# Kernel optimization log

Measured on AMD Instinct MI355X. Metric: run time of the kernel, lower is better.

Reference implementation:

```python
import jax, jax.numpy as jnp
import numpy as np

N, C, H, W = 8, 64, 128, 128
K2 = 9  # 3x3 kernel
BN_EPS = 1e-5


def conv3x3(x, w):
    # x: [N,Ci,H,W], w: [Co,Ci,3,3], stride 1, padding 1, dilation 1
    return jax.lax.conv_general_dilated(
        x, w, window_strides=(1, 1), padding=((1, 1), (1, 1)),
        dimension_numbers=('NCHW', 'OIHW', 'NCHW'))


def deform_conv3x3(x, offset, w):
    # torchvision deform_conv2d v1 (no mask), stride 1, pad 1, dil 1, 1 group.
    # offset: [N, 2*K2, H, W] ordered (dy, dx) per kernel tap.
    n, c, h, wd = x.shape
    off = offset.reshape(n, K2, 2, h, wd)
    k = jnp.arange(3) - 1  # kernel tap displacements with pad=1
    ky, kx = jnp.meshgrid(k, k, indexing='ij')
    ky = ky.reshape(K2).astype(x.dtype)
    kx = kx.reshape(K2).astype(x.dtype)
    ys = jnp.arange(h, dtype=x.dtype)
    xs = jnp.arange(wd, dtype=x.dtype)
    # sampling positions: [N, K2, H, W]
    py = ys[None, None, :, None] + ky[None, :, None, None] + off[:, :, 0]
    px = xs[None, None, None, :] + kx[None, :, None, None] + off[:, :, 1]
    y0f = jnp.floor(py)
    x0f = jnp.floor(px)
    wy1 = py - y0f
    wx1 = px - x0f
    y0 = y0f.astype(jnp.int32)
    x0 = x0f.astype(jnp.int32)
    xflat = x.reshape(n, c, h * wd)

    def corner(yc, xc, wgt):
        valid = ((yc >= 0) & (yc < h) & (xc >= 0) & (xc < wd)).astype(x.dtype)
        idx = jnp.clip(yc, 0, h - 1) * wd + jnp.clip(xc, 0, wd - 1)  # [N,K2,H,W]
        gath = jax.vmap(lambda xf, i: jnp.take(xf, i.reshape(-1), axis=1)
                        .reshape(c, K2, h, wd))(xflat, idx)  # [N,C,K2,H,W]
        return gath * (wgt * valid)[:, None]

    samp = (corner(y0, x0, (1 - wy1) * (1 - wx1))
            + corner(y0, x0 + 1, (1 - wy1) * wx1)
            + corner(y0 + 1, x0, wy1 * (1 - wx1))
            + corner(y0 + 1, x0 + 1, wy1 * wx1))  # [N,C,K2,H,W]
    return jnp.einsum('nckhw,ock->nohw', samp, w.reshape(w.shape[0], c, K2))


def setup_inputs() -> dict:
    key = jax.random.key(0)
    ks = jax.random.split(key, 5)
    x = jax.random.normal(ks[0], (N, C, H, W), dtype=jnp.float32)
    # small offset-conv weights so predicted offsets stay within a few pixels
    w_off = jax.random.normal(ks[1], (2 * K2 + 9, C, 3, 3), dtype=jnp.float32) * 0.01
    w_def = jax.random.normal(ks[2], (C, C, 3, 3), dtype=jnp.float32) * (1.0 / np.sqrt(C * 9))
    w1 = jax.random.normal(ks[3], (K2, C, 3, 3), dtype=jnp.float32) * (1.0 / np.sqrt(C * 9))
    gamma = jnp.ones((K2,), jnp.float32)
    beta = jnp.zeros((K2,), jnp.float32)
    mean = jnp.zeros((K2,), jnp.float32)
    var = jnp.ones((K2,), jnp.float32)
    return {"x": x, "w_off": w_off, "w_def": w_def, "w1": w1,
            "gamma": gamma, "beta": beta, "mean": mean, "var": var}


def reference(x, w_off, w_def, w1, gamma, beta, mean, var):
    off_filter = conv3x3(x, w_off)            # [N, 27, H, W]
    offset = off_filter[:, :2 * K2]           # [N, 18, H, W]
    filt = off_filter[:, -K2:]                # [N, 9, H, W]
    out = deform_conv3x3(x, offset, w_def)    # [N, C, H, W]
    xr = x + out
    h = conv3x3(xr, w1)                       # [N, 9, H, W]
    # BatchNorm2d (inference form with running stats)
    h = (h - mean[None, :, None, None]) * jax.lax.rsqrt(var[None, :, None, None] + BN_EPS)
    h = h * gamma[None, :, None, None] + beta[None, :, None, None]
    h = jnp.maximum(h, 0.0)
    return (h, filt)
```

## Files before the change

kernel.cpp:

```cpp
#include <hip/hip_runtime.h>
#include <cmath>

#define H_ 128
#define W_ 128
#define HW_ 16384
#define C_ 64
#define N_ 8
#define BN_EPS 1e-5f

typedef __attribute__((ext_vector_type(8))) short short8;
typedef __attribute__((ext_vector_type(4))) float float4_;

__device__ inline short f2bf(float f) {
    unsigned u = __builtin_bit_cast(unsigned, f);
    u += 0x7fffu + ((u >> 16) & 1u);
    return (short)(u >> 16);
}
__device__ inline float bf2f(short s) {
    unsigned u = ((unsigned)(unsigned short)s) << 16;
    return __builtin_bit_cast(float, u);
}

#define OFFB_OFS   0
#define XB8_OFS    9437184
#define XR8_OFS    26214400
#define WDEFB_OFS  42991616
#define BT27_OFS   43065344
#define BT9_OFS    43102720

__global__ __launch_bounds__(256) void prep_w(
    const float* __restrict__ w_off, const float* __restrict__ w_def,
    const float* __restrict__ w1, short* __restrict__ wdefB,
    short* __restrict__ bt27, short* __restrict__ bt9)
{
    int i = blockIdx.x * 256 + threadIdx.x;
    if (i < 36864) {
        int o = i / 576, r = i - o*576, t = r >> 6, c = r & 63;
        wdefB[i] = f2bf(w_def[o*576 + c*9 + t]);
    } else if (i < 36864 + 18688) {
        int j = i - 36864;
        int oc = j / 584, K = j - oc*584;
        float v = 0.f;
        if (oc < 27 && K < 576) { int t = K >> 6, c = K & 63; v = w_off[oc*576 + c*9 + t]; }
        bt27[j] = f2bf(v);
    } else if (i < 36864 + 18688 + 9344) {
        int j = i - 36864 - 18688;
        int oc = j / 584, K = j - oc*584;
        float v = 0.f;
        if (oc < 9 && K < 576) { int t = K >> 6, c = K & 63; v = w1[oc*576 + c*9 + t]; }
        bt9[j] = f2bf(v);
    }
}

__global__ __launch_bounds__(256) void convert_x(
    const float* __restrict__ x, short8* __restrict__ xb8)
{
    int idx = blockIdx.x * 256 + threadIdx.x;
    int pix = idx & (HW_-1);
    int c8  = (idx >> 14) & 7;
    int n   = idx >> 17;
    const float* xp = x + ((size_t)(n*64 + c8*8))*HW_ + pix;
    short8 v;
    #pragma unroll
    for (int j = 0; j < 8; j++) v[j] = f2bf(xp[j*HW_]);
    xb8[idx] = v;
}

__global__ __launch_bounds__(256) void conv27_mfma(
    const short8* __restrict__ xb8, const short* __restrict__ bt_g,
    float* __restrict__ off_buf, float* __restrict__ filt_out)
{
    __shared__ short8 patch[8*325];
    __shared__ short8 btl[32*73];
    const int tid = threadIdx.x;
    const int bx = blockIdx.x, by = blockIdx.y, n = blockIdx.z;

    for (int i = tid; i < 2336; i += 256) btl[i] = ((const short8*)bt_g)[i];
    for (int i = tid; i < 2592; i += 256) {
        int c8 = i / 324, r = i - c8*324;
        int py = r / 18, px = r - py*18;
        int gy = by*16 - 1 + py, gx = bx*16 - 1 + px;
        short8 v = {0,0,0,0,0,0,0,0};
        if ((unsigned)gy < 128u && (unsigned)gx < 128u)
            v = xb8[(size_t)(n*8 + c8)*HW_ + gy*W_ + gx];
        patch[c8*325 + py*18 + px] = v;
    }
    __syncthreads();

    const int lane = tid & 63, wid = tid >> 6;
    const int q = lane >> 4, col = lane & 15;
    float4_ acc[4][2];
    #pragma unroll
    for (int i = 0; i < 4; i++) {
        acc[i][0] = (float4_){0.f,0.f,0.f,0.f};
        acc[i][1] = (float4_){0.f,0.f,0.f,0.f};
    }

    #pragma unroll 2
    for (int k0 = 0; k0 < 18; k0++) {
        int t = k0 >> 1;
        int dy = t/3, dx = t - dy*3;
        int c8 = (k0 & 1)*4 + q;
        short8 b0 = btl[col*73 + k0*4 + q];
        short8 b1 = btl[(16 + col)*73 + k0*4 + q];
        #pragma unroll
        for (int i = 0; i < 4; i++) {
            int mt = wid*4 + i;
            short8 a = patch[c8*325 + (mt + dy)*18 + (col + dx)];
            acc[i][0] = __builtin_amdgcn_mfma_f32_16x16x32_bf16(a, b0, acc[i][0], 0,0,0);
            acc[i][1] = __builtin_amdgcn_mfma_f32_16x16x32_bf16(a, b1, acc[i][1], 0,0,0);
        }
    }

    #pragma unroll
    for (int i = 0; i < 4; i++) {
        int ty = wid*4 + i;
        #pragma unroll
        for (int nt = 0; nt < 2; nt++) {
            int oc = nt*16 + col;
            if (oc >= 27) continue;
            #pragma unroll
            for (int reg = 0; reg < 4; reg++) {
                int tx = q*4 + reg;
                int pix = (by*16 + ty)*W_ + bx*16 + tx;
                float v = acc[i][nt][reg];
                if (oc < 18) off_buf[((size_t)n*18 + oc)*HW_ + pix] = v;
                else         filt_out[((size_t)n*9 + (oc-18))*HW_ + pix] = v;
            }
        }
    }
}

__global__ __launch_bounds__(256, 2) void deform_mfma(
    const float* __restrict__ off_buf, const short8* __restrict__ xb8,
    const short8* __restrict__ wdefB, short* __restrict__ xr8s)
{
    const int tid = threadIdx.x;
    const int bx = blockIdx.x, by = blockIdx.y, n = blockIdx.z;
    const int lane = tid & 63, wid = tid >> 6;
    const int q = lane >> 4, col = lane & 15;
    const float*  ob    = off_buf + (size_t)n*18*HW_;
    const short8* xbase = xb8 + (size_t)n*8*HW_;
    const short*  xbs   = (const short*)xbase;

    float4_ acc[4][4];
    #pragma unroll
    for (int i = 0; i < 4; i++)
        #pragma unroll
        for (int nt = 0; nt < 4; nt++) acc[i][nt] = (float4_){0.f,0.f,0.f,0.f};

    #pragma unroll 1
    for (int t = 0; t < 9; t++) {
        const int dy = t/3 - 1, dx = t - (t/3)*3 - 1;
        short8 afrag[4][2];
        #pragma unroll
        for (int i = 0; i < 4; i++) {
            const int gy = by*16 + wid*4 + i;
            const int gx = bx*16 + col;
            const int pix = gy*W_ + gx;
            float offy = ob[(2*t)*HW_ + pix];
            float offx = ob[(2*t+1)*HW_ + pix];
            float py = (float)(gy + dy) + offy;
            float px = (float)(gx + dx) + offx;
            float y0f = floorf(py), x0f = floorf(px);
            float wy1 = py - y0f, wx1 = px - x0f;
            float wy0 = 1.f - wy1, wx0 = 1.f - wx1;
            int y0 = (int)y0f, x0 = (int)x0f;
            int y1 = y0 + 1,   x1 = x0 + 1;
            float vy0 = ((unsigned)y0 < (unsigned)H_) ? 1.f : 0.f;
            float vy1 = ((unsigned)y1 < (unsigned)H_) ? 1.f : 0.f;
            float vx0 = ((unsigned)x0 < (unsigned)W_) ? 1.f : 0.f;
            float vx1 = ((unsigned)x1 < (unsigned)W_) ? 1.f : 0.f;
            float w00 = wy0*wx0*vy0*vx0, w01 = wy0*wx1*vy0*vx1;
            float w10 = wy1*wx0*vy1*vx0, w11 = wy1*wx1*vy1*vx1;
            int cy0 = min(max(y0, 0), H_-1), cy1 = min(max(y1, 0), H_-1);
            int cx0 = min(max(x0, 0), W_-1), cx1 = min(max(x1, 0), W_-1);
            int i00 = cy0*W_ + cx0, i01 = cy0*W_ + cx1;
            int i10 = cy1*W_ + cx0, i11 = cy1*W_ + cx1;
            #pragma unroll
            for (int ks = 0; ks < 2; ks++) {
                const short8* xg = xbase + (size_t)(ks*4 + q)*HW_;
                short8 p00 = xg[i00], p01 = xg[i01];
                short8 p10 = xg[i10], p11 = xg[i11];
                short8 a;
                #pragma unroll
                for (int j = 0; j < 8; j++) {
                    float s = bf2f(p00[j])*w00 + bf2f(p01[j])*w01
                            + bf2f(p10[j])*w10 + bf2f(p11[j])*w11;
                    a[j] = f2bf(s);
                }
                afrag[i][ks] = a;
            }
        }
        #pragma unroll
        for (int ks = 0; ks < 2; ks++) {
            #pragma unroll
            for (int nt = 0; nt < 4; nt++) {
                short8 b = wdefB[(size_t)(nt*16 + col)*72 + t*8 + ks*4 + q];
                #pragma unroll
                for (int i = 0; i < 4; i++)
                    acc[i][nt] = __builtin_amdgcn_mfma_f32_16x16x32_bf16(
                        afrag[i][ks], b, acc[i][nt], 0,0,0);
            }
        }
    }

    short* xout = xr8s + (size_t)n*8*HW_*8;
    #pragma unroll
    for (int i = 0; i < 4; i++) {
        const int gy = by*16 + wid*4 + i;
        #pragma unroll
        for (int nt = 0; nt < 4; nt++) {
            const int o = nt*16 + col;
            #pragma unroll
            for (int reg = 0; reg < 4; reg++) {
                const int gx = bx*16 + q*4 + reg;
                const int pix = gy*W_ + gx;
                size_t si = ((size_t)(o >> 3)*HW_ + pix)*8 + (o & 7);
                float r = bf2f(xbs[si]);
                xout[si] = f2bf(acc[i][nt][reg] + r);
            }
        }
    }
}

__global__ __launch_bounds__(256) void conv9_mfma(
    const short8* __restrict__ xr8, const short* __restrict__ bt_g,
    const float* __restrict__ gamma, const float* __restrict__ beta,
    const float* __restrict__ mean, const float* __restrict__ var,
    float* __restrict__ out)
{
    __shared__ short8 patch[8*325];
    __shared__ short8 btl[16*73];
    const int tid = threadIdx.x;
    const int bx = blockIdx.x, by = blockIdx.y, n = blockIdx.z;

    for (int i = tid; i < 1168; i += 256) btl[i] = ((const short8*)bt_g)[i];
    for (int i = tid; i < 2592; i += 256) {
        int c8 = i / 324, r = i - c8*324;
        int py = r / 18, px = r - py*18;
        int gy = by*16 - 1 + py, gx = bx*16 - 1 + px;
        short8 v = {0,0,0,0,0,0,0,0};
        if ((unsigned)gy < 128u && (unsigned)gx < 128u)
            v = xr8[(size_t)(n*8 + c8)*HW_ + gy*W_ + gx];
        patch[c8*325 + py*18 + px] = v;
    }
    __syncthreads();

    const int lane = tid & 63, wid = tid >> 6;
    const int q = lane >> 4, col = lane & 15;
    float4_ acc[4];
    #pragma unroll
    for (int i = 0; i < 4; i++) acc[i] = (float4_){0.f,0.f,0.f,0.f};

    #pragma unroll 2
    for (int k0 = 0; k0 < 18; k0++) {
        int t = k0 >> 1;
        int dy = t/3, dx = t - dy*3;
        int c8 = (k0 & 1)*4 + q;
        short8 b0 = btl[col*73 + k0*4 + q];
        #pragma unroll
        for (int i = 0; i < 4; i++) {
            int mt = wid*4 + i;
            short8 a = patch[c8*325 + (mt + dy)*18 + (col + dx)];
            acc[i] = __builtin_amdgcn_mfma_f32_16x16x32_bf16(a, b0, acc[i], 0,0,0);
        }
    }

    float sc = 0.f, sh = 0.f;
    if (col < 9) {
        sc = gamma[col] * rsqrtf(var[col] + BN_EPS);
        sh = beta[col] - mean[col] * sc;
    }
    #pragma unroll
    for (int i = 0; i < 4; i++) {
        int ty = wid*4 + i;
        if (col < 9) {
            #pragma unroll
            for (int reg = 0; reg < 4; reg++) {
                int tx = q*4 + reg;
                int pix = (by*16 + ty)*W_ + bx*16 + tx;
                float h = fmaxf(fmaf(acc[i][reg], sc, sh), 0.f);
                out[((size_t)n*9 + col)*HW_ + pix] = h;
            }
        }
    }
}

extern "C" void kernel_launch(void* const* d_in, const int* in_sizes, int n_in,
                              void* d_out, int out_size, void* d_ws, size_t ws_size,
                              hipStream_t stream)
{
    const float* x     = (const float*)d_in[0];
    const float* w_off = (const float*)d_in[1];
    const float* w_def = (const float*)d_in[2];
    const float* w1    = (const float*)d_in[3];
    const float* gamma = (const float*)d_in[4];
    const float* beta  = (const float*)d_in[5];
    const float* mean  = (const float*)d_in[6];
    const float* var   = (const float*)d_in[7];
    float* out = (float*)d_out;

    char* ws = (char*)d_ws;
    float*  off_buf = (float*)(ws + OFFB_OFS);
    short8* xb8     = (short8*)(ws + XB8_OFS);
    short8* xr8     = (short8*)(ws + XR8_OFS);
    short*  wdefB   = (short*)(ws + WDEFB_OFS);
    short*  bt27    = (short*)(ws + BT27_OFS);
    short*  bt9     = (short*)(ws + BT9_OFS);

    float* h_out    = out;
    float* filt_out = out + (size_t)N_ * 9 * HW_;

    prep_w<<<dim3(254), dim3(256), 0, stream>>>(w_off, w_def, w1, wdefB, bt27, bt9);
    convert_x<<<dim3(4096), dim3(256), 0, stream>>>(x, xb8);

    dim3 cgrid(8, 8, 8);
    conv27_mfma<<<cgrid, dim3(256), 0, stream>>>(xb8, bt27, off_buf, filt_out);
    deform_mfma<<<cgrid, dim3(256), 0, stream>>>(off_buf, xb8, (const short8*)wdefB, (short*)xr8);
    conv9_mfma<<<cgrid, dim3(256), 0, stream>>>(xr8, bt9, gamma, beta, mean, var, h_out);
}
```

Before: 190.7 us.

## Stage input halo patch in LDS for deformable bilinear gathers and prefetch offsets

Each block loads a 22x22 halo patch of all 64 bf16 channels into shared memory, and bilinear corner reads come from LDS when the sampled coordinates fall inside the patch. Otherwise they fall back to global memory. Offsets for the next tap are prefetched one iteration ahead to hide global load latency. The aim is to replace scattered global gathers with LDS reads. In exchange, the block uses about 62KB of LDS, which may limit occupancy to fewer blocks per CU, and adds a divergent branch.

```diff
diff --git a/kernel.cpp b/kernel.cpp
--- a/kernel.cpp
+++ b/kernel.cpp
@@ -135,33 +135,59 @@
     const float* __restrict__ off_buf, const short8* __restrict__ xb8,
     const short8* __restrict__ wdefB, short* __restrict__ xr8s)
 {
+    __shared__ short8 patch[8*484];
     const int tid = threadIdx.x;
     const int bx = blockIdx.x, by = blockIdx.y, n = blockIdx.z;
     const int lane = tid & 63, wid = tid >> 6;
     const int q = lane >> 4, col = lane & 15;
+    const int r0 = by*16 - 3, c0 = bx*16 - 3;
     const float*  ob    = off_buf + (size_t)n*18*HW_;
     const short8* xbase = xb8 + (size_t)n*8*HW_;
     const short*  xbs   = (const short*)xbase;
 
+    for (int i = tid; i < 3872; i += 256) {
+        int c8 = i / 484, r = i - c8*484;
+        int py = r / 22, px = r - py*22;
+        int gy = r0 + py, gx = c0 + px;
+        short8 v = {0,0,0,0,0,0,0,0};
+        if ((unsigned)gy < 128u && (unsigned)gx < 128u)
+            v = xbase[(size_t)c8*HW_ + gy*W_ + gx];
+        patch[c8*484 + r] = v;
+    }
+    __syncthreads();
+
+    const int gxc = bx*16 + col;
+    int pixi[4];
+    #pragma unroll
+    for (int i = 0; i < 4; i++) pixi[i] = (by*16 + wid*4 + i)*W_ + gxc;
+
     float4_ acc[4][4];
     #pragma unroll
     for (int i = 0; i < 4; i++)
         #pragma unroll
         for (int nt = 0; nt < 4; nt++) acc[i][nt] = (float4_){0.f,0.f,0.f,0.f};
+
+    float oy[4], ox[4];
+    #pragma unroll
+    for (int i = 0; i < 4; i++) { oy[i] = ob[pixi[i]]; ox[i] = ob[HW_ + pixi[i]]; }
 
     #pragma unroll 1
     for (int t = 0; t < 9; t++) {
-        const int dy = t/3 - 1, dx = t - (t/3)*3 - 1;
+        const int dy = t/3 - 1, dx = (t - (t/3)*3) - 1;
+        float oyn[4], oxn[4];
+        if (t < 8) {
+            #pragma unroll
+            for (int i = 0; i < 4; i++) {
+                oyn[i] = ob[(2*t+2)*HW_ + pixi[i]];
+                oxn[i] = ob[(2*t+3)*HW_ + pixi[i]];
+            }
+        }
         short8 afrag[4][2];
         #pragma unroll
         for (int i = 0; i < 4; i++) {
             const int gy = by*16 + wid*4 + i;
-            const int gx = bx*16 + col;
-            const int pix = gy*W_ + gx;
-            float offy = ob[(2*t)*HW_ + pix];
-            float offx = ob[(2*t+1)*HW_ + pix];
-            float py = (float)(gy + dy) + offy;
-            float px = (float)(gx + dx) + offx;
+            float py = (float)(gy + dy) + oy[i];
+            float px = (float)(gxc + dx) + ox[i];
             float y0f = floorf(py), x0f = floorf(px);
             float wy1 = py - y0f, wx1 = px - x0f;
             float wy0 = 1.f - wy1, wx0 = 1.f - wx1;
@@ -175,13 +201,23 @@
             float w10 = wy1*wx0*vy1*vx0, w11 = wy1*wx1*vy1*vx1;
             int cy0 = min(max(y0, 0), H_-1), cy1 = min(max(y1, 0), H_-1);
             int cx0 = min(max(x0, 0), W_-1), cx1 = min(max(x1, 0), W_-1);
-            int i00 = cy0*W_ + cx0, i01 = cy0*W_ + cx1;
-            int i10 = cy1*W_ + cx0, i11 = cy1*W_ + cx1;
+            int ly0 = cy0 - r0, ly1 = cy1 - r0;
+            int lx0 = cx0 - c0, lx1 = cx1 - c0;
+            bool inp = ((unsigned)ly0 < 22u) & ((unsigned)ly1 < 22u)
+                     & ((unsigned)lx0 < 22u) & ((unsigned)lx1 < 22u);
             #pragma unroll
             for (int ks = 0; ks < 2; ks++) {
-                const short8* xg = xbase + (size_t)(ks*4 + q)*HW_;
-                short8 p00 = xg[i00], p01 = xg[i01];
-                short8 p10 = xg[i10], p11 = xg[i11];
+                const int c8 = ks*4 + q;
+                short8 p00, p01, p10, p11;
+                if (inp) {
+                    const short8* pl = &patch[c8*484];
+                    p00 = pl[ly0*22 + lx0]; p01 = pl[ly0*22 + lx1];
+                    p10 = pl[ly1*22 + lx0]; p11 = pl[ly1*22 + lx1];
+                } else {
+                    const short8* xg = xbase + (size_t)c8*HW_;
+                    p00 = xg[cy0*W_ + cx0]; p01 = xg[cy0*W_ + cx1];
+                    p10 = xg[cy1*W_ + cx0]; p11 = xg[cy1*W_ + cx1];
+                }
                 short8 a;
                 #pragma unroll
                 for (int j = 0; j < 8; j++) {
@@ -203,6 +239,8 @@
                         afrag[i][ks], b, acc[i][nt], 0,0,0);
             }
         }
+        #pragma unroll
+        for (int i = 0; i < 4; i++) { oy[i] = oyn[i]; ox[i] = oxn[i]; }
     }
 
     short* xout = xr8s + (size_t)n*8*HW_*8;
```

New measurement: 172.0 us. 9.8% less time.

## Fuse x conversion, offset conv and deformable conv into one kernel

Applied to the files above, without the earlier changes.

Removes the separate convert_x and conv27 kernels. A single kernel now loads a 20x20 bf16 halo patch of x straight from fp32 into LDS, computes the offset conv with MFMA, keeps the offsets in shared memory, and samples bilinear corners from the LDS patch. Samples that land outside the patch fall back to global fp32 reads. This drops the off_buf and xb8 round trips through global memory and two launches. The cost is more LDS per block, a possible divergent slow path for large offsets, and vectorized float4 output stores.

```diff
diff --git a/kernel.cpp b/kernel.cpp
--- a/kernel.cpp
+++ b/kernel.cpp
@@ -21,12 +21,13 @@
     return __builtin_bit_cast(float, u);
 }
 
-#define OFFB_OFS   0
-#define XB8_OFS    9437184
-#define XR8_OFS    26214400
-#define WDEFB_OFS  42991616
-#define BT27_OFS   43065344
-#define BT9_OFS    43102720
+#define XR8_OFS    0
+#define WDEFB_OFS  16777216
+#define BT27_OFS   16850944
+#define BT9_OFS    16888320
+
+#define PS_ 402
+#define OS_ 260
 
 __global__ __launch_bounds__(256) void prep_w(
     const float* __restrict__ w_off, const float* __restrict__ w_def,
@@ -52,96 +53,72 @@
     }
 }
 
-__global__ __launch_bounds__(256) void convert_x(
-    const float* __restrict__ x, short8* __restrict__ xb8)
+__global__ __launch_bounds__(256, 2) void fused_off_deform(
+    const float* __restrict__ x, const short8* __restrict__ btg27,
+    const short8* __restrict__ wdefB, float* __restrict__ filt_out,
+    short* __restrict__ xr8s)
 {
-    int idx = blockIdx.x * 256 + threadIdx.x;
-    int pix = idx & (HW_-1);
-    int c8  = (idx >> 14) & 7;
-    int n   = idx >> 17;
-    const float* xp = x + ((size_t)(n*64 + c8*8))*HW_ + pix;
-    short8 v;
-    #pragma unroll
-    for (int j = 0; j < 8; j++) v[j] = f2bf(xp[j*HW_]);
-    xb8[idx] = v;
-}
-
-__global__ __launch_bounds__(256) void conv27_mfma(
-    const short8* __restrict__ xb8, const short* __restrict__ bt_g,
-    float* __restrict__ off_buf, float* __restrict__ filt_out)
-{
-    __shared__ short8 patch[8*325];
-    __shared__ short8 btl[32*73];
-    const int tid = threadIdx.x;
-    const int bx = blockIdx.x, by = blockIdx.y, n = blockIdx.z;
-
-    for (int i = tid; i < 2336; i += 256) btl[i] = ((const short8*)bt_g)[i];
-    for (int i = tid; i < 2592; i += 256) {
-        int c8 = i / 324, r = i - c8*324;
-        int py = r / 18, px = r - py*18;
-        int gy = by*16 - 1 + py, gx = bx*16 - 1 + px;
-        short8 v = {0,0,0,0,0,0,0,0};
-        if ((unsigned)gy < 128u && (unsigned)gx < 128u)
-            v = xb8[(size_t)(n*8 + c8)*HW_ + gy*W_ + gx];
-        patch[c8*325 + py*18 + px] = v;
-    }
-    __syncthreads();
-
-    const int lane = tid & 63, wid = tid >> 6;
-    const int q = lane >> 4, col = lane & 15;
-    float4_ acc[4][2];
-    #pragma unroll
-    for (int i = 0; i < 4; i++) {
-        acc[i][0] = (float4_){0.f,0.f,0.f,0.f};
-        acc[i][1] = (float4_){0.f,0.f,0.f,0.f};
-    }
-
-    #pragma unroll 2
-    for (int k0 = 0; k0 < 18; k0++) {
-        int t = k0 >> 1;
-        int dy = t/3, dx = t - dy*3;
-        int c8 = (k0 & 1)*4 + q;
-        short8 b0 = btl[col*73 + k0*4 + q];
-        short8 b1 = btl[(16 + col)*73 + k0*4 + q];
-        #pragma unroll
-        for (int i = 0; i < 4; i++) {
-            int mt = wid*4 + i;
-            short8 a = patch[c8*325 + (mt + dy)*18 + (col + dx)];
-            acc[i][0] = __builtin_amdgcn_mfma_f32_16x16x32_bf16(a, b0, acc[i][0], 0,0,0);
-            acc[i][1] = __builtin_amdgcn_mfma_f32_16x16x32_bf16(a, b1, acc[i][1], 0,0,0);
-        }
-    }
-
-    #pragma unroll
-    for (int i = 0; i < 4; i++) {
-        int ty = wid*4 + i;
-        #pragma unroll
-        for (int nt = 0; nt < 2; nt++) {
-            int oc = nt*16 + col;
-            if (oc >= 27) continue;
-            #pragma unroll
-            for (int reg = 0; reg < 4; reg++) {
-                int tx = q*4 + reg;
-                int pix = (by*16 + ty)*W_ + bx*16 + tx;
-                float v = acc[i][nt][reg];
-                if (oc < 18) off_buf[((size_t)n*18 + oc)*HW_ + pix] = v;
-                else         filt_out[((size_t)n*9 + (oc-18))*HW_ + pix] = v;
-            }
-        }
-    }
-}
-
-__global__ __launch_bounds__(256, 2) void deform_mfma(
-    const float* __restrict__ off_buf, const short8* __restrict__ xb8,
-    const short8* __restrict__ wdefB, short* __restrict__ xr8s)
-{
+    __shared__ short8 patch[8*PS_];
+    __shared__ float  offs[18*OS_];
     const int tid = threadIdx.x;
     const int bx = blockIdx.x, by = blockIdx.y, n = blockIdx.z;
     const int lane = tid & 63, wid = tid >> 6;
     const int q = lane >> 4, col = lane & 15;
-    const float*  ob    = off_buf + (size_t)n*18*HW_;
-    const short8* xbase = xb8 + (size_t)n*8*HW_;
-    const short*  xbs   = (const short*)xbase;
+    const int r0 = by*16 - 2, c0 = bx*16 - 2;
+    const float* xb = x + (size_t)n * C_ * HW_;
+
+    for (int i = tid; i < 3200; i += 256) {
+        int c8 = i / 400, r = i - c8*400;
+        int py = r / 20, px = r - py*20;
+        int gy = r0 + py, gx = c0 + px;
+        short8 v = {0,0,0,0,0,0,0,0};
+        if ((unsigned)gy < 128u && (unsigned)gx < 128u) {
+            const float* xp = xb + (size_t)(c8*8)*HW_ + gy*W_ + gx;
+            #pragma unroll
+            for (int j = 0; j < 8; j++) v[j] = f2bf(xp[j*HW_]);
+        }
+        patch[c8*PS_ + py*20 + px] = v;
+    }
+    __syncthreads();
+
+    {
+        float4_ a27[4][2];
+        #pragma unroll
+        for (int i = 0; i < 4; i++) {
+            a27[i][0] = (float4_){0.f,0.f,0.f,0.f};
+            a27[i][1] = (float4_){0.f,0.f,0.f,0.f};
+        }
+        #pragma unroll 2
+        for (int k0 = 0; k0 < 18; k0++) {
+            int t = k0 >> 1;
+            int dy = t/3, dx = t - dy*3;
+            int c8 = (k0 & 1)*4 + q;
+            short8 b0 = btg27[col*73 + k0*4 + q];
+            short8 b1 = btg27[(16 + col)*73 + k0*4 + q];
+            #pragma unroll
+            for (int i = 0; i < 4; i++) {
+                int mt = wid*4 + i;
+                short8 a = patch[c8*PS_ + (mt + dy + 1)*20 + (col + dx + 1)];
+                a27[i][0] = __builtin_amdgcn_mfma_f32_16x16x32_bf16(a, b0, a27[i][0], 0,0,0);
+                a27[i][1] = __builtin_amdgcn_mfma_f32_16x16x32_bf16(a, b1, a27[i][1], 0,0,0);
+            }
+        }
+        #pragma unroll
+        for (int i = 0; i < 4; i++) {
+            int mt = wid*4 + i;
+            #pragma unroll
+            for (int nt = 0; nt < 2; nt++) {
+                int oc = nt*16 + col;
+                if (oc < 18) {
+                    *(float4_*)&offs[oc*OS_ + mt*16 + q*4] = a27[i][nt];
+                } else if (oc < 27) {
+                    int pix0 = (by*16 + mt)*W_ + bx*16 + q*4;
+                    *(float4_*)&filt_out[((size_t)n*9 + (oc-18))*HW_ + pix0] = a27[i][nt];
+                }
+            }
+        }
+    }
+    __syncthreads();
 
     float4_ acc[4][4];
     #pragma unroll
@@ -151,17 +128,16 @@
 
     #pragma unroll 1
     for (int t = 0; t < 9; t++) {
-        const int dy = t/3 - 1, dx = t - (t/3)*3 - 1;
+        const int dy = t/3 - 1, dx = (t - (t/3)*3) - 1;
         short8 afrag[4][2];
         #pragma unroll
         for (int i = 0; i < 4; i++) {
-            const int gy = by*16 + wid*4 + i;
-            const int gx = bx*16 + col;
-            const int pix = gy*W_ + gx;
-            float offy = ob[(2*t)*HW_ + pix];
-            float offx = ob[(2*t+1)*HW_ + pix];
-            float py = (float)(gy + dy) + offy;
-            float px = (float)(gx + dx) + offx;
+            const int row = wid*4 + i;
+            const int gy = by*16 + row, gxc = bx*16 + col;
+            float oy = offs[(2*t)*OS_ + row*16 + col];
+            float ox = offs[(2*t+1)*OS_ + row*16 + col];
+            float py = (float)(gy + dy) + oy;
+            float px = (float)(gxc + dx) + ox;
             float y0f = floorf(py), x0f = floorf(px);
             float wy1 = py - y0f, wx1 = px - x0f;
             float wy0 = 1.f - wy1, wx0 = 1.f - wx1;
@@ -175,19 +151,33 @@
             float w10 = wy1*wx0*vy1*vx0, w11 = wy1*wx1*vy1*vx1;
             int cy0 = min(max(y0, 0), H_-1), cy1 = min(max(y1, 0), H_-1);
             int cx0 = min(max(x0, 0), W_-1), cx1 = min(max(x1, 0), W_-1);
-            int i00 = cy0*W_ + cx0, i01 = cy0*W_ + cx1;
-            int i10 = cy1*W_ + cx0, i11 = cy1*W_ + cx1;
+            int ly0 = cy0 - r0, ly1 = cy1 - r0;
+            int lx0 = cx0 - c0, lx1 = cx1 - c0;
+            bool inp = ((unsigned)ly0 < 20u) & ((unsigned)ly1 < 20u)
+                     & ((unsigned)lx0 < 20u) & ((unsigned)lx1 < 20u);
             #pragma unroll
             for (int ks = 0; ks < 2; ks++) {
-                const short8* xg = xbase + (size_t)(ks*4 + q)*HW_;
-                short8 p00 = xg[i00], p01 = xg[i01];
-                short8 p10 = xg[i10], p11 = xg[i11];
+                const int c8 = ks*4 + q;
                 short8 a;
-                #pragma unroll
-                for (int j = 0; j < 8; j++) {
-                    float s = bf2f(p00[j])*w00 + bf2f(p01[j])*w01
-                            + bf2f(p10[j])*w10 + bf2f(p11[j])*w11;
-                    a[j] = f2bf(s);
+                if (inp) {
+                    const short8* pl = &patch[c8*PS_];
+                    short8 p00 = pl[ly0*20 + lx0], p01 = pl[ly0*20 + lx1];
+                    short8 p10 = pl[ly1*20 + lx0], p11 = pl[ly1*20 + lx1];
+                    #pragma unroll
+                    for (int j = 0; j < 8; j++) {
+                        float s = bf2f(p00[j])*w00 + bf2f(p01[j])*w01
+                                + bf2f(p10[j])*w10 + bf2f(p11[j])*w11;
+                        a[j] = f2bf(s);
+                    }
+                } else {
+                    const float* xg = xb + (size_t)(c8*8)*HW_;
+                    #pragma unroll
+                    for (int j = 0; j < 8; j++) {
+                        const float* xj = xg + (size_t)j*HW_;
+                        float s = xj[cy0*W_+cx0]*w00 + xj[cy0*W_+cx1]*w01
+                                + xj[cy1*W_+cx0]*w10 + xj[cy1*W_+cx1]*w11;
+                        a[j] = f2bf(s);
+                    }
                 }
                 afrag[i][ks] = a;
             }
@@ -205,20 +195,21 @@
         }
     }
 
+    const short* ps = (const short*)patch;
     short* xout = xr8s + (size_t)n*8*HW_*8;
     #pragma unroll
     for (int i = 0; i < 4; i++) {
-        const int gy = by*16 + wid*4 + i;
+        const int row = wid*4 + i;
+        const int gy = by*16 + row;
         #pragma unroll
         for (int nt = 0; nt < 4; nt++) {
             const int o = nt*16 + col;
             #pragma unroll
             for (int reg = 0; reg < 4; reg++) {
-                const int gx = bx*16 + q*4 + reg;
-                const int pix = gy*W_ + gx;
-                size_t si = ((size_t)(o >> 3)*HW_ + pix)*8 + (o & 7);
-                float r = bf2f(xbs[si]);
-                xout[si] = f2bf(acc[i][nt][reg] + r);
+                const int m = q*4 + reg;
+                const int pix = gy*W_ + bx*16 + m;
+                float r = bf2f(ps[(((o>>3)*PS_ + (row+2)*20 + (m+2)) << 3) + (o & 7)]);
+                xout[((size_t)(o>>3)*HW_ + pix)*8 + (o & 7)] = f2bf(acc[i][nt][reg] + r);
             }
         }
     }
@@ -274,15 +265,14 @@
     }
     #pragma unroll
     for (int i = 0; i < 4; i++) {
-        int ty = wid*4 + i;
+        int mt = wid*4 + i;
         if (col < 9) {
-            #pragma unroll
-            for (int reg = 0; reg < 4; reg++) {
-                int tx = q*4 + reg;
-                int pix = (by*16 + ty)*W_ + bx*16 + tx;
-                float h = fmaxf(fmaf(acc[i][reg], sc, sh), 0.f);
-                out[((size_t)n*9 + col)*HW_ + pix] = h;
-            }
+            int pix0 = (by*16 + mt)*W_ + bx*16 + q*4;
+            float4_ v;
+            #pragma unroll
+            for (int reg = 0; reg < 4; reg++)
+                v[reg] = fmaxf(fmaf(acc[i][reg], sc, sh), 0.f);
+            *(float4_*)&out[((size_t)n*9 + col)*HW_ + pix0] = v;
         }
     }
 }
@@ -302,8 +292,6 @@
     float* out = (float*)d_out;
 
     char* ws = (char*)d_ws;
-    float*  off_buf = (float*)(ws + OFFB_OFS);
-    short8* xb8     = (short8*)(ws + XB8_OFS);
     short8* xr8     = (short8*)(ws + XR8_OFS);
     short*  wdefB   = (short*)(ws + WDEFB_OFS);
     short*  bt27    = (short*)(ws + BT27_OFS);
@@ -313,10 +301,9 @@
     float* filt_out = out + (size_t)N_ * 9 * HW_;
 
     prep_w<<<dim3(254), dim3(256), 0, stream>>>(w_off, w_def, w1, wdefB, bt27, bt9);
-    convert_x<<<dim3(4096), dim3(256), 0, stream>>>(x, xb8);
 
     dim3 cgrid(8, 8, 8);
-    conv27_mfma<<<cgrid, dim3(256), 0, stream>>>(xb8, bt27, off_buf, filt_out);
-    deform_mfma<<<cgrid, dim3(256), 0, stream>>>(off_buf, xb8, (const short8*)wdefB, (short*)xr8);
+    fused_off_deform<<<cgrid, dim3(256), 0, stream>>>(
+        x, (const short8*)bt27, (const short8*)wdefB, filt_out, (short*)xr8);
     conv9_mfma<<<cgrid, dim3(256), 0, stream>>>(xr8, bt9, gamma, beta, mean, var, h_out);
 }
```

After: 163.0 us. -14.5%, faster.
